# Kernel optimization log

Hardware: AMD Instinct MI355X
Metric: run time of the kernel (lower is better)

## Reference

```python
import jax, jax.numpy as jnp
from jax import lax
import numpy as np

IMG = 15      # odd spatial edge; num_patches = 4*(IMG-1) = 56
CH = 256      # spectral channels
DIM = 512
HEADS = 8
DH = 64       # dim_head; inner_dim = HEADS*DH = 512
DEPTH = 6
MLP = 2048
NCLS = 16
RATIO = 0.5   # args.ratio (scalar, not trainable)
SCALE = DH ** -0.5
NPATCH = 4 * (IMG - 1)


def _ring(a1, a2, b1, b2, E, mid1, mid2):
    # Exact replica of outer_sampling traversal; returns static index tables.
    tgt, s1, s2 = [], [], []
    d = [0, 1]; l1 = a1; l2 = b1 - 1; start = 0
    while True:
        l1 += d[0]; l2 += d[1]
        if l1 == a1 and l2 == b1:
            if start == 1:
                break
            start = 1
        if l1 > a2:
            d = [0, -1]; l1 -= 1; continue
        elif l2 < b1:
            d = [-1, 0]; l2 += 1; continue
        elif l2 > b2:
            d = [1, 0]; l2 -= 1; continue
        if l1 < 0 or l1 > E or l2 < 0 or l2 > E:
            continue
        m1 = 0 if l1 == mid1 else -int(np.sign(l1 - mid1))
        m2 = 0 if l2 == mid2 else -int(np.sign(l2 - mid2))
        if abs(l1 - mid1) > abs(l2 - mid2):
            s1.append((l1 + m1) * E + l2); s2.append((l1 + m1) * E + l2 + m2)
        elif abs(l1 - mid1) < abs(l2 - mid2):
            s1.append(l1 * E + l2 + m2); s2.append((l1 + m1) * E + l2 + m2)
        else:  # corner: x[t] += ratio * x[s] == (x[s]+x[s])*ratio/2
            s = (l1 + m1) * E + l2 + m2
            s1.append(s); s2.append(s)
        tgt.append(l1 * E + l2)
    return np.array(tgt), np.array(s1), np.array(s2)

_MID = IMG // 2
# Within each ring, every read hits an already-finalized inner-ring cell,
# so rings can be applied as vectorized gather+scatter in sequence.
RINGS = [_ring(_MID - i, _MID + i, _MID - i, _MID + i, IMG, _MID, _MID)
         for i in range(1, _MID + 1)]


def _sinusoid(n_pos, d):
    pos = np.arange(n_pos)[:, None].astype(np.float64)
    j = np.arange(d)[None, :]
    ang = pos / np.power(10000.0, 2 * (j // 2) / d)
    tab = np.zeros((n_pos, d))
    tab[:, 0::2] = np.sin(ang[:, 0::2])
    tab[:, 1::2] = np.cos(ang[:, 1::2])
    return jnp.asarray(tab[None], dtype=jnp.float32)

POS = _sinusoid(NPATCH + 1, DIM)


def _ln(x, g, b, eps=1e-5):
    mu = x.mean(-1, keepdims=True)
    v = ((x - mu) ** 2).mean(-1, keepdims=True)
    return (x - mu) * lax.rsqrt(v + eps) * g + b


def _forward(x, We, be, cls_token, Wqkv, Wo, bo, ln1g, ln1b, W1, b1, W2, b2,
             ln2g, ln2b, lnh_g, lnh_b, Wh, bh):
    B = x.shape[0]
    xf = x.reshape(B, CH, IMG * IMG)
    for tgt, s1, s2 in RINGS:
        xf = xf.at[:, :, tgt].set(xf[:, :, tgt] + (xf[:, :, s1] + xf[:, :, s2]) * (RATIO / 2))
    # original runs spiral under torch.no_grad()
    tok = lax.stop_gradient(jnp.transpose(xf[:, :, RINGS[-1][0]], (0, 2, 1)))  # [B, 56, CH]
    h = tok @ We + be                                                          # [B, 56, DIM]
    h = jnp.concatenate([jnp.broadcast_to(cls_token, (B, 1, DIM)), h], axis=1)
    h = h + POS[:, :NPATCH + 1]
    for l in range(DEPTH):
        y = _ln(h, ln1g[l], ln1b[l])
        qkv = y @ Wqkv[l]
        q, k, v = [t.reshape(B, -1, HEADS, DH).transpose(0, 2, 1, 3)
                   for t in jnp.split(qkv, 3, axis=-1)]
        a = jax.nn.softmax(jnp.einsum('bhid,bhjd->bhij', q, k) * SCALE, axis=-1)
        o = jnp.einsum('bhij,bhjd->bhid', a, v).transpose(0, 2, 1, 3).reshape(B, -1, HEADS * DH)
        h = h + o @ Wo[l] + bo[l]
        y = _ln(h, ln2g[l], ln2b[l])
        h = h + jax.nn.gelu(y @ W1[l] + b1[l], approximate=False) @ W2[l] + b2[l]
    p = h.mean(axis=1)  # pool='mean'
    return _ln(p, lnh_g, lnh_b) @ Wh + bh


def setup_inputs():
    key = jax.random.key(0)
    ks = jax.random.split(key, 8)
    B = 512
    def nrm(k, shp, s=0.02):
        return jax.random.normal(k, shp, jnp.float32) * s
    return {
        'x': jax.random.normal(ks[0], (B, CH, IMG, IMG), jnp.float32),
        'We': nrm(ks[1], (CH, DIM)),
        'be': jnp.zeros((DIM,), jnp.float32),
        'cls_token': nrm(ks[2], (1, 1, DIM), 1.0),
        'Wqkv': nrm(ks[3], (DEPTH, DIM, 3 * HEADS * DH)),
        'Wo': nrm(ks[4], (DEPTH, HEADS * DH, DIM)),
        'bo': jnp.zeros((DEPTH, DIM), jnp.float32),
        'ln1g': jnp.ones((DEPTH, DIM), jnp.float32),
        'ln1b': jnp.zeros((DEPTH, DIM), jnp.float32),
        'W1': nrm(ks[5], (DEPTH, DIM, MLP)),
        'b1': jnp.zeros((DEPTH, MLP), jnp.float32),
        'W2': nrm(ks[6], (DEPTH, MLP, DIM)),
        'b2': jnp.zeros((DEPTH, DIM), jnp.float32),
        'ln2g': jnp.ones((DEPTH, DIM), jnp.float32),
        'ln2b': jnp.zeros((DEPTH, DIM), jnp.float32),
        'lnh_g': jnp.ones((DIM,), jnp.float32),
        'lnh_b': jnp.zeros((DIM,), jnp.float32),
        'Wh': nrm(ks[7], (DIM, NCLS)),
        'bh': jnp.zeros((NCLS,), jnp.float32),
    }


def reference(x, We, be, cls_token, Wqkv, Wo, bo, ln1g, ln1b, W1, b1, W2, b2,
              ln2g, ln2b, lnh_g, lnh_b, Wh, bh):
    return _forward(x, We, be, cls_token, Wqkv, Wo, bo, ln1g, ln1b, W1, b1,
                    W2, b2, ln2g, ln2b, lnh_g, lnh_b, Wh, bh)
```

## Files before the change

kernel.cpp:

```cpp
#include <hip/hip_runtime.h>
#include <math.h>

#define NB   512
#define SEQ  57
#define NP   56
#define CHN  256
#define DIM  512
#define MLPD 2048

typedef float f32x4 __attribute__((ext_vector_type(4)));
typedef short s16x8 __attribute__((ext_vector_type(8)));

__device__ __forceinline__ short f2bf(float f) {
    union { float f; unsigned u; } v; v.f = f;
    unsigned r = (v.u + 0x7fffu + ((v.u >> 16) & 1u)) >> 16;
    return (short)r;
}
__device__ __forceinline__ float geluf(float v) {
    return 0.5f * v * (1.0f + erff(v * 0.70710678118654752f));
}

#define GLDS16(g, l) __builtin_amdgcn_global_load_lds(                         \
    (const __attribute__((address_space(1))) void*)(g),                        \
    (__attribute__((address_space(3))) void*)(l), 16, 0, 0)

struct RingTables { int tgt[224]; int s1[224]; int s2[224]; int start[8]; };
constexpr RingTables make_rings() {
    RingTables rt{};
    int n = 0; const int E = 15, mid = 7;
    rt.start[0] = 0;
    for (int i = 1; i <= 7; ++i) {
        int a1 = mid - i, a2 = mid + i, b1 = mid - i, b2 = mid + i;
        int d0 = 0, d1 = 1, l1 = a1, l2 = b1 - 1, started = 0;
        while (true) {
            l1 += d0; l2 += d1;
            if (l1 == a1 && l2 == b1) { if (started) break; started = 1; }
            if (l1 > a2)      { d0 = 0;  d1 = -1; l1 -= 1; continue; }
            else if (l2 < b1) { d0 = -1; d1 = 0;  l2 += 1; continue; }
            else if (l2 > b2) { d0 = 1;  d1 = 0;  l2 -= 1; continue; }
            if (l1 < 0 || l1 > E || l2 < 0 || l2 > E) continue;
            int m1 = -((l1 > mid) - (l1 < mid));
            int m2 = -((l2 > mid) - (l2 < mid));
            int ab1 = l1 > mid ? l1 - mid : mid - l1;
            int ab2 = l2 > mid ? l2 - mid : mid - l2;
            if (ab1 > ab2)      { rt.s1[n] = (l1+m1)*E + l2;   rt.s2[n] = (l1+m1)*E + l2+m2; }
            else if (ab1 < ab2) { rt.s1[n] = l1*E + l2+m2;     rt.s2[n] = (l1+m1)*E + l2+m2; }
            else                { int s = (l1+m1)*E + l2+m2;   rt.s1[n] = s; rt.s2[n] = s; }
            rt.tgt[n] = l1*E + l2;
            ++n;
        }
        rt.start[i] = n;
    }
    return rt;
}
constexpr RingTables RT_HOST = make_rings();
__constant__ RingTables RT = RT_HOST;

__global__ __launch_bounds__(256) void spiral_kernel(const float* __restrict__ x,
                                                     short* __restrict__ tok) {
    __shared__ float tile[64 * 225];
    const int b  = blockIdx.x >> 2;
    const int c0 = (blockIdx.x & 3) << 6;
    const float* src = x + ((size_t)b * CHN + c0) * 225;
    for (int i = threadIdx.x; i < 64 * 225; i += 256) tile[i] = src[i];
    __syncthreads();
    for (int r = 0; r < 7; ++r) {
        const int s0 = RT.start[r], n = RT.start[r + 1] - s0;
        for (int w = threadIdx.x; w < (n << 6); w += 256) {
            const int c = w & 63, t = s0 + (w >> 6);
            float* row = tile + c * 225;
            row[RT.tgt[t]] += (row[RT.s1[t]] + row[RT.s2[t]]) * 0.25f;
        }
        __syncthreads();
    }
    for (int w = threadIdx.x; w < (56 << 6); w += 256) {
        const int c = w & 63, p = w >> 6;
        tok[((size_t)b * NP + p) * CHN + c0 + c] = f2bf(tile[c * 225 + RT.tgt[168 + p]]);
    }
}

__global__ __launch_bounds__(256) void transcvt(const float* __restrict__ in,
                                                short* __restrict__ out, int K, int N) {
    __shared__ float t[32][33];
    in  += (size_t)blockIdx.z * K * N;
    out += (size_t)blockIdx.z * K * N;
    const int k0 = blockIdx.y << 5, n0 = blockIdx.x << 5;
    const int tx = threadIdx.x & 31, ty = threadIdx.x >> 5;
    for (int i = ty; i < 32; i += 8) t[i][tx] = in[(size_t)(k0 + i) * N + n0 + tx];
    __syncthreads();
    for (int i = ty; i < 32; i += 8) out[(size_t)(n0 + i) * K + k0 + tx] = f2bf(t[tx][i]);
}

__global__ __launch_bounds__(256) void pos_kernel(float* __restrict__ pos) {
    const int idx = blockIdx.x * 256 + threadIdx.x;
    const int t = idx >> 9, j = idx & 511;
    double expo = (double)(2 * (j >> 1)) / 512.0;
    double ang  = (double)t * pow(10000.0, -expo);
    pos[idx] = (j & 1) ? (float)cos(ang) : (float)sin(ang);
}

__global__ __launch_bounds__(256) void assemble_kernel(const float* __restrict__ emb,
                                                       const float* __restrict__ cls,
                                                       const float* __restrict__ pos,
                                                       float* __restrict__ h) {
    const unsigned idx = blockIdx.x * 256 + threadIdx.x;
    const int c = idx & 511;
    const int r = (idx >> 9) % SEQ;
    const unsigned b = idx / (SEQ * DIM);
    float base = (r == 0) ? cls[c] : emb[((size_t)b * NP + (r - 1)) * DIM + c];
    h[idx] = base + pos[r * DIM + c];
}

__global__ __launch_bounds__(256) void ln_kernel(const float* __restrict__ x,
                                                 const float* __restrict__ g,
                                                 const float* __restrict__ bta,
                                                 short* __restrict__ y) {
    const int row  = (blockIdx.x << 2) + (threadIdx.x >> 6);
    const int lane = threadIdx.x & 63;
    const float* xr = x + (size_t)row * DIM;
    float v[8]; float s = 0.f;
#pragma unroll
    for (int j = 0; j < 8; ++j) { v[j] = xr[lane + (j << 6)]; s += v[j]; }
#pragma unroll
    for (int off = 1; off < 64; off <<= 1) s += __shfl_xor(s, off);
    const float mu = s * (1.f / 512.f);
    float sq = 0.f;
#pragma unroll
    for (int j = 0; j < 8; ++j) { const float d = v[j] - mu; sq += d * d; }
#pragma unroll
    for (int off = 1; off < 64; off <<= 1) sq += __shfl_xor(sq, off);
    const float rs = rsqrtf(sq * (1.f / 512.f) + 1e-5f);
    short* yr = y + (size_t)row * DIM;
#pragma unroll
    for (int j = 0; j < 8; ++j) {
        const int c = lane + (j << 6);
        yr[c] = f2bf((v[j] - mu) * rs * g[c] + bta[c]);
    }
}

template<int ACT, bool RES, bool OUTBF>
__global__ __launch_bounds__(256, 2) void gemm_bf16(
    const short* __restrict__ A, const short* __restrict__ BT,
    const float* __restrict__ bias, const float* __restrict__ res,
    void* __restrict__ Cout, int M, int N, int K)
{
    __shared__ short As[128 * 32];
    __shared__ short Bs[128 * 32];
    const int tid = threadIdx.x;
    const int m0 = blockIdx.y << 7, n0 = blockIdx.x << 7;
    const int wave = tid >> 6, lane = tid & 63;
    const int wm = (wave >> 1) << 6, wn = (wave & 1) << 6;
    const int fm = lane & 15, fq = lane >> 4;

    const int g0 = (wave << 7) + lane;
    const int r0 = g0 >> 2, c0 = (g0 & 3) << 3;
    const int g1 = g0 + 64;
    const int r1 = g1 >> 2, c1 = (g1 & 3) << 3;

    const short* Ap0 = A  + (size_t)(m0 + r0) * K + c0;
    const short* Ap1 = A  + (size_t)(m0 + r1) * K + c1;
    const short* Bp0 = BT + (size_t)(n0 + r0) * K + c0;
    const short* Bp1 = BT + (size_t)(n0 + r1) * K + c1;
    short* lA0 = As + (size_t)((wave << 7) + 0 ) * 8;
    short* lA1 = As + (size_t)((wave << 7) + 64) * 8;
    short* lB0 = Bs + (size_t)((wave << 7) + 0 ) * 8;
    short* lB1 = Bs + (size_t)((wave << 7) + 64) * 8;

    f32x4 acc[4][4] = {};

    for (int k0 = 0; k0 < K; k0 += 32) {
        __syncthreads();
        GLDS16(Ap0 + k0, lA0);
        GLDS16(Ap1 + k0, lA1);
        GLDS16(Bp0 + k0, lB0);
        GLDS16(Bp1 + k0, lB1);
        __syncthreads();
        s16x8 af[4], bfr[4];
#pragma unroll
        for (int s = 0; s < 4; ++s) {
            af[s]  = *(const s16x8*)(As + (wm + s * 16 + fm) * 32 + (fq << 3));
            bfr[s] = *(const s16x8*)(Bs + (wn + s * 16 + fm) * 32 + (fq << 3));
        }
#pragma unroll
        for (int i = 0; i < 4; ++i)
#pragma unroll
            for (int j = 0; j < 4; ++j)
                acc[i][j] = __builtin_amdgcn_mfma_f32_16x16x32_bf16(af[i], bfr[j], acc[i][j], 0, 0, 0);
    }

#pragma unroll
    for (int i = 0; i < 4; ++i) {
#pragma unroll
        for (int r = 0; r < 4; ++r) {
            const int row = m0 + wm + i * 16 + (fq << 2) + r;
#pragma unroll
            for (int j = 0; j < 4; ++j) {
                const int col = n0 + wn + j * 16 + fm;
                float v = acc[i][j][r];
                if (bias) v += bias[col];
                if (ACT == 1) v = geluf(v);
                if (RES) v += res[(size_t)row * N + col];
                if (OUTBF) ((short*)Cout)[(size_t)row * N + col] = f2bf(v);
                else       ((float*)Cout)[(size_t)row * N + col] = v;
            }
        }
    }
}

__global__ __launch_bounds__(64) void attn_mfma(const short* __restrict__ qkv,
                                                short* __restrict__ o) {
    __shared__ short Pl[64 * 72];
    __shared__ short Vt[64 * 72];
    const int b = blockIdx.x >> 3, hd = blockIdx.x & 7;
    const int lane = threadIdx.x;
    const int n = lane & 15, q = lane >> 4;
    const short* base = qkv + (size_t)b * SEQ * 1536 + hd * 64;

    {
        const short* vb = base + 1024 + lane;
        for (int t = 0; t < SEQ; ++t) Vt[lane * 72 + t] = vb[(size_t)t * 1536];
        for (int t = SEQ; t < 64; ++t) Vt[lane * 72 + t] = 0;
    }

    const s16x8 zero8 = {};
    s16x8 qf[4][2], kf[4][2];
#pragma unroll
    for (int ti = 0; ti < 4; ++ti) {
        const int tq = ti * 16 + n;
#pragma unroll
        for (int kk = 0; kk < 2; ++kk) {
            const int ko = kk * 32 + q * 8;
            qf[ti][kk] = (tq < SEQ) ? *(const s16x8*)(base + (size_t)tq * 1536 + ko)       : zero8;
            kf[ti][kk] = (tq < SEQ) ? *(const s16x8*)(base + 512 + (size_t)tq * 1536 + ko) : zero8;
        }
    }

    f32x4 sacc[4][4] = {};
#pragma unroll
    for (int ti = 0; ti < 4; ++ti)
#pragma unroll
        for (int tj = 0; tj < 4; ++tj)
#pragma unroll
            for (int kk = 0; kk < 2; ++kk)
                sacc[ti][tj] = __builtin_amdgcn_mfma_f32_16x16x32_bf16(
                    qf[ti][kk], kf[tj][kk], sacc[ti][tj], 0, 0, 0);

#pragma unroll
    for (int ti = 0; ti < 4; ++ti) {
#pragma unroll
        for (int r = 0; r < 4; ++r) {
            float v[4]; float mx = -1e30f;
#pragma unroll
            for (int tj = 0; tj < 4; ++tj) {
                float s = sacc[ti][tj][r] * 0.125f;
                if (tj * 16 + n >= SEQ) s = -1e30f;
                v[tj] = s; mx = fmaxf(mx, s);
            }
            mx = fmaxf(mx, __shfl_xor(mx, 1));
            mx = fmaxf(mx, __shfl_xor(mx, 2));
            mx = fmaxf(mx, __shfl_xor(mx, 4));
            mx = fmaxf(mx, __shfl_xor(mx, 8));
            float sum = 0.f;
#pragma unroll
            for (int tj = 0; tj < 4; ++tj) { v[tj] = __expf(v[tj] - mx); sum += v[tj]; }
            sum += __shfl_xor(sum, 1); sum += __shfl_xor(sum, 2);
            sum += __shfl_xor(sum, 4); sum += __shfl_xor(sum, 8);
            const float inv = 1.f / sum;
            const int row = ti * 16 + q * 4 + r;
#pragma unroll
            for (int tj = 0; tj < 4; ++tj)
                Pl[row * 72 + tj * 16 + n] = f2bf(v[tj] * inv);
        }
    }
    __syncthreads();

    f32x4 oacc[4][4] = {};
#pragma unroll
    for (int kk = 0; kk < 2; ++kk) {
        s16x8 pf[4], vf[4];
#pragma unroll
        for (int s = 0; s < 4; ++s) {
            pf[s] = *(const s16x8*)(Pl + (s * 16 + n) * 72 + kk * 32 + q * 8);
            vf[s] = *(const s16x8*)(Vt + (s * 16 + n) * 72 + kk * 32 + q * 8);
        }
#pragma unroll
        for (int ti = 0; ti < 4; ++ti)
#pragma unroll
            for (int td = 0; td < 4; ++td)
                oacc[ti][td] = __builtin_amdgcn_mfma_f32_16x16x32_bf16(
                    pf[ti], vf[td], oacc[ti][td], 0, 0, 0);
    }
#pragma unroll
    for (int ti = 0; ti < 4; ++ti) {
#pragma unroll
        for (int r = 0; r < 4; ++r) {
            const int trow = ti * 16 + q * 4 + r;
            if (trow < SEQ) {
#pragma unroll
                for (int td = 0; td < 4; ++td)
                    o[((size_t)(b * SEQ + trow)) * DIM + hd * 64 + td * 16 + n]
                        = f2bf(oacc[ti][td][r]);
            }
        }
    }
}

__global__ __launch_bounds__(256) void head_kernel(const float* __restrict__ h,
                                                   const float* __restrict__ g,
                                                   const float* __restrict__ bb,
                                                   const float* __restrict__ Wh,
                                                   const float* __restrict__ bh,
                                                   float* __restrict__ out) {
    __shared__ float p[DIM];
    __shared__ float r1[4], r2[4];
    const int b = blockIdx.x;
    const float* hb = h + (size_t)b * SEQ * DIM;
    for (int c = threadIdx.x; c < DIM; c += 256) {
        float s = 0.f;
        for (int t = 0; t < SEQ; ++t) s += hb[t * DIM + c];
        p[c] = s * (1.f / 57.f);
    }
    __syncthreads();
    float s = 0.f;
    for (int c = threadIdx.x; c < DIM; c += 256) s += p[c];
#pragma unroll
    for (int off = 1; off < 64; off <<= 1) s += __shfl_xor(s, off);
    if ((threadIdx.x & 63) == 0) r1[threadIdx.x >> 6] = s;
    __syncthreads();
    const float mu = (r1[0] + r1[1] + r1[2] + r1[3]) * (1.f / 512.f);
    float sq = 0.f;
    for (int c = threadIdx.x; c < DIM; c += 256) { float d = p[c] - mu; sq += d * d; }
#pragma unroll
    for (int off = 1; off < 64; off <<= 1) sq += __shfl_xor(sq, off);
    if ((threadIdx.x & 63) == 0) r2[threadIdx.x >> 6] = sq;
    __syncthreads();
    const float rs = rsqrtf((r2[0] + r2[1] + r2[2] + r2[3]) * (1.f / 512.f) + 1e-5f);
    for (int c = threadIdx.x; c < DIM; c += 256) p[c] = (p[c] - mu) * rs * g[c] + bb[c];
    __syncthreads();
    if (threadIdx.x < 16) {
        float acc = bh[threadIdx.x];
        for (int c = 0; c < DIM; ++c) acc += p[c] * Wh[c * 16 + threadIdx.x];
        out[b * 16 + threadIdx.x] = acc;
    }
}

extern "C" void kernel_launch(void* const* d_in, const int* in_sizes, int n_in,
                              void* d_out, int out_size, void* d_ws, size_t ws_size,
                              hipStream_t stream) {
    (void)in_sizes; (void)n_in; (void)out_size; (void)ws_size;
    const float* x    = (const float*)d_in[0];
    const float* We   = (const float*)d_in[1];
    const float* be   = (const float*)d_in[2];
    const float* cls  = (const float*)d_in[3];
    const float* Wqkv = (const float*)d_in[4];
    const float* Wo   = (const float*)d_in[5];
    const float* bo   = (const float*)d_in[6];
    const float* ln1g = (const float*)d_in[7];
    const float* ln1b = (const float*)d_in[8];
    const float* W1   = (const float*)d_in[9];
    const float* b1   = (const float*)d_in[10];
    const float* W2   = (const float*)d_in[11];
    const float* b2   = (const float*)d_in[12];
    const float* ln2g = (const float*)d_in[13];
    const float* ln2b = (const float*)d_in[14];
    const float* lnhg = (const float*)d_in[15];
    const float* lnhb = (const float*)d_in[16];
    const float* Wh   = (const float*)d_in[17];
    const float* bh   = (const float*)d_in[18];

    char* ws = (char*)d_ws;
    float* h    = (float*)(ws);
    float* big  = (float*)(ws + 59768832);
    short* bigs = (short*)big;
    short* ybf  = (short*)(ws + 239075328);
    short* wbuf = (short*)(ws + 268959744);
    short* tokb = (short*)(ws + 306970624);
    float* pos  = (float*)(ws + 321650688);

    short* WeT   = wbuf;
    short* WqkvT = wbuf + 131072;
    short* WoT   = WqkvT + 6 * 786432;
    short* W1T   = WoT   + 6 * 262144;
    short* W2T   = W1T   + 6 * 1048576;

    pos_kernel<<<114, 256, 0, stream>>>(pos);
    transcvt<<<dim3(16,  8, 1), 256, 0, stream>>>(We,   WeT,    256,  512);
    transcvt<<<dim3(48, 16, 6), 256, 0, stream>>>(Wqkv, WqkvT,  512, 1536);
    transcvt<<<dim3(16, 16, 6), 256, 0, stream>>>(Wo,   WoT,    512,  512);
    transcvt<<<dim3(64, 16, 6), 256, 0, stream>>>(W1,   W1T,    512, 2048);
    transcvt<<<dim3(16, 64, 6), 256, 0, stream>>>(W2,   W2T,   2048,  512);
    spiral_kernel<<<2048, 256, 0, stream>>>(x, tokb);

    gemm_bf16<0, false, false><<<dim3(4, 224), 256, 0, stream>>>(
        tokb, WeT, be, nullptr, big, NB * NP, DIM, CHN);
    assemble_kernel<<<(NB * SEQ * DIM) / 256, 256, 0, stream>>>(big, cls, pos, h);

    const int M = NB * SEQ;
    for (int l = 0; l < 6; ++l) {
        ln_kernel<<<M / 4, 256, 0, stream>>>(h, ln1g + l * 512, ln1b + l * 512, ybf);
        gemm_bf16<0, false, true><<<dim3(12, 228), 256, 0, stream>>>(
            ybf, WqkvT + (size_t)l * 786432, nullptr, nullptr, bigs, M, 1536, 512);
        attn_mfma<<<NB * 8, 64, 0, stream>>>(bigs, ybf);
        gemm_bf16<0, true, false><<<dim3(4, 228), 256, 0, stream>>>(
            ybf, WoT + (size_t)l * 262144, bo + l * 512, h, h, M, 512, 512);
        ln_kernel<<<M / 4, 256, 0, stream>>>(h, ln2g + l * 512, ln2b + l * 512, ybf);
        gemm_bf16<1, false, true><<<dim3(16, 228), 256, 0, stream>>>(
            ybf, W1T + (size_t)l * 1048576, b1 + l * 2048, nullptr, bigs, M, 2048, 512);
        gemm_bf16<0, true, false><<<dim3(4, 228), 256, 0, stream>>>(
            bigs, W2T + (size_t)l * 1048576, b2 + l * 512, h, h, M, 512, 2048);
    }
    head_kernel<<<NB, 256, 0, stream>>>(h, lnhg, lnhb, Wh, bh, (float*)d_out);
}
```

Before: 2.917 ms.

## Double GEMM K-tile to 64 and XOR-swizzle LDS layout

The bf16 GEMM now stages a 64-wide K slice per iteration instead of 32, which halves the number of barrier pairs per tile. The LDS layout is XOR-swizzled on the global source column so that MFMA fragment reads avoid bank conflicts. LDS use per block doubles to 32 KB, which may reduce occupancy, and the loop now assumes K is a multiple of 64.

```diff
diff --git a/kernel.cpp b/kernel.cpp
--- a/kernel.cpp
+++ b/kernel.cpp
@@ -144,48 +144,51 @@
     const float* __restrict__ bias, const float* __restrict__ res,
     void* __restrict__ Cout, int M, int N, int K)
 {
-    __shared__ short As[128 * 32];
-    __shared__ short Bs[128 * 32];
+    __shared__ short As[128 * 64];
+    __shared__ short Bs[128 * 64];
     const int tid = threadIdx.x;
     const int m0 = blockIdx.y << 7, n0 = blockIdx.x << 7;
     const int wave = tid >> 6, lane = tid & 63;
     const int wm = (wave >> 1) << 6, wn = (wave & 1) << 6;
     const int fm = lane & 15, fq = lane >> 4;
 
-    const int g0 = (wave << 7) + lane;
-    const int r0 = g0 >> 2, c0 = (g0 & 3) << 3;
-    const int g1 = g0 + 64;
-    const int r1 = g1 >> 2, c1 = (g1 & 3) << 3;
-
-    const short* Ap0 = A  + (size_t)(m0 + r0) * K + c0;
-    const short* Ap1 = A  + (size_t)(m0 + r1) * K + c1;
-    const short* Bp0 = BT + (size_t)(n0 + r0) * K + c0;
-    const short* Bp1 = BT + (size_t)(n0 + r1) * K + c1;
-    short* lA0 = As + (size_t)((wave << 7) + 0 ) * 8;
-    short* lA1 = As + (size_t)((wave << 7) + 64) * 8;
-    short* lB0 = Bs + (size_t)((wave << 7) + 0 ) * 8;
-    short* lB1 = Bs + (size_t)((wave << 7) + 64) * 8;
+    const short* Ap[4]; const short* Bp[4];
+    short *lA[4], *lB[4];
+#pragma unroll
+    for (int t = 0; t < 4; ++t) {
+        const int g = t * 256 + tid;
+        const int row = g >> 3;
+        const int c = (g & 7) ^ (row & 7);
+        Ap[t] = A  + (size_t)(m0 + row) * K + (c << 3);
+        Bp[t] = BT + (size_t)(n0 + row) * K + (c << 3);
+        lA[t] = As + g * 8;
+        lB[t] = Bs + g * 8;
+    }
 
     f32x4 acc[4][4] = {};
 
-    for (int k0 = 0; k0 < K; k0 += 32) {
+    for (int k0 = 0; k0 < K; k0 += 64) {
         __syncthreads();
-        GLDS16(Ap0 + k0, lA0);
-        GLDS16(Ap1 + k0, lA1);
-        GLDS16(Bp0 + k0, lB0);
-        GLDS16(Bp1 + k0, lB1);
+#pragma unroll
+        for (int t = 0; t < 4; ++t) GLDS16(Ap[t] + k0, lA[t]);
+#pragma unroll
+        for (int t = 0; t < 4; ++t) GLDS16(Bp[t] + k0, lB[t]);
         __syncthreads();
-        s16x8 af[4], bfr[4];
-#pragma unroll
-        for (int s = 0; s < 4; ++s) {
-            af[s]  = *(const s16x8*)(As + (wm + s * 16 + fm) * 32 + (fq << 3));
-            bfr[s] = *(const s16x8*)(Bs + (wn + s * 16 + fm) * 32 + (fq << 3));
-        }
-#pragma unroll
-        for (int i = 0; i < 4; ++i)
-#pragma unroll
-            for (int j = 0; j < 4; ++j)
-                acc[i][j] = __builtin_amdgcn_mfma_f32_16x16x32_bf16(af[i], bfr[j], acc[i][j], 0, 0, 0);
+#pragma unroll
+        for (int kk = 0; kk < 2; ++kk) {
+            const int cs = ((fq + (kk << 2)) ^ (fm & 7)) << 3;
+            s16x8 af[4], bfr[4];
+#pragma unroll
+            for (int s = 0; s < 4; ++s) {
+                af[s]  = *(const s16x8*)(As + (wm + s * 16 + fm) * 64 + cs);
+                bfr[s] = *(const s16x8*)(Bs + (wn + s * 16 + fm) * 64 + cs);
+            }
+#pragma unroll
+            for (int i = 0; i < 4; ++i)
+#pragma unroll
+                for (int j = 0; j < 4; ++j)
+                    acc[i][j] = __builtin_amdgcn_mfma_f32_16x16x32_bf16(af[i], bfr[j], acc[i][j], 0, 0, 0);
+        }
     }
 
 #pragma unroll
```

Result: faster. 2.694 ms (-7.6%).
